# Kernel optimization log

Measured on AMD Instinct MI355X. Metric: run time of the kernel, lower is better.

The kernel has to match this reference:

```python
import jax, jax.numpy as jnp
import numpy as np

N = 50000
E = 500000
H = 128


def _linear(x, w, b):
    # torch nn.Linear: y = x @ W.T + b, W is [out, in]
    return x @ w.T + b


def _layer(x, h, edge_index, w0_w, w0_b, wl_w, wl_b, w1_w, w1_b):
    # PyG MessagePassing(aggr='add', flow='target_to_source'):
    # x_j = h[edge_index[1]], scatter-add into edge_index[0], dim_size = N
    msg = h[edge_index[1]]                               # [E, H] gather
    aggr = jax.ops.segment_sum(msg, edge_index[0], num_segments=h.shape[0])  # [N, H]
    return _linear(aggr, wl_w, wl_b) + _linear(h, w0_w, w0_b) + _linear(x, w1_w, w1_b)


def setup_inputs() -> dict:
    key = jax.random.key(0)
    ks = jax.random.split(key, 12)
    wscale = 0.05
    return {
        "x_a": jax.random.normal(ks[0], (N, H), jnp.float32),
        "x_b": jax.random.normal(ks[1], (N, H), jnp.float32),
        "edge_ab": jax.random.randint(ks[2], (2, E), 0, N, jnp.int32),
        "edge_ba": jax.random.randint(ks[3], (2, E), 0, N, jnp.int32),
        "conv0_w0_w": jax.random.normal(ks[4], (H, H), jnp.float32) * wscale,
        "conv0_w0_b": jnp.zeros((H,), jnp.float32),
        "conv0_wl_w": jax.random.normal(ks[5], (H, H), jnp.float32) * wscale,
        "conv0_wl_b": jnp.zeros((H,), jnp.float32),
        "conv0_w1_w": jax.random.normal(ks[6], (H, H), jnp.float32) * wscale,
        "conv0_w1_b": jnp.zeros((H,), jnp.float32),
        "conv1_w0_w": jax.random.normal(ks[7], (H, H), jnp.float32) * wscale,
        "conv1_w0_b": jnp.zeros((H,), jnp.float32),
        "conv1_wl_w": jax.random.normal(ks[8], (H, H), jnp.float32) * wscale,
        "conv1_wl_b": jnp.zeros((H,), jnp.float32),
        "conv1_w1_w": jax.random.normal(ks[9], (H, H), jnp.float32) * wscale,
        "conv1_w1_b": jnp.zeros((H,), jnp.float32),
        "out_w": jax.random.normal(ks[10], (H, H), jnp.float32) * wscale,
        "out_b": jnp.zeros((H,), jnp.float32),
    }


def reference(x_a, x_b, edge_ab, edge_ba,
              conv0_w0_w, conv0_w0_b, conv0_wl_w, conv0_wl_b, conv0_w1_w, conv0_w1_b,
              conv1_w0_w, conv1_w0_b, conv1_wl_w, conv1_wl_b, conv1_w1_w, conv1_w1_b,
              out_w, out_b):
    # metapath = [(a, r1, b), (b, r2, a)], loop over reversed(metapath):
    # iter 0: conv_idx=1, edge (b, r2, a), dst='a'
    h_a = jax.nn.relu(_layer(x_a, x_a, edge_ba,
                             conv1_w0_w, conv1_w0_b, conv1_wl_w, conv1_wl_b, conv1_w1_w, conv1_w1_b))
    # iter 1: conv_idx=0, edge (a, r1, b), dst='b'
    h_b = jax.nn.relu(_layer(x_b, x_b, edge_ab,
                             conv0_w0_w, conv0_w0_b, conv0_wl_w, conv0_wl_b, conv0_w1_w, conv0_w1_b))
    # start_type = 'a'
    return _linear(h_a, out_w, out_b)
```

## Files before the change

kernel.cpp:

```cpp
#include <hip/hip_runtime.h>
#include <hip/hip_bf16.h>

#define NN 50000
#define NE 500000
#define HD 128
#define CAP 128
#define PREP_B 24
#define ZCUR_B ((NN + 255) / 256)
#define ZAGGR_B 6250
#define K1_B (PREP_B + ZCUR_B + ZAGGR_B)
#define FILLB_B ((NE + 255) / 256)
#define XCONV_B 3125
#define K2_B (FILLB_B + XCONV_B)

typedef __bf16 bf16;
typedef __attribute__((ext_vector_type(8))) __bf16 bf16x8;
typedef __attribute__((ext_vector_type(4))) float floatx4;

__device__ inline float u2f(unsigned int lo16) {
    union { unsigned int i; float f; } c; c.i = lo16 << 16; return c.f;
}

__device__ inline bf16x8 cvt8(floatx4 a, floatx4 b) {
    bf16x8 r;
#pragma unroll
    for (int j = 0; j < 4; j++) { r[j] = (bf16)a[j]; r[j + 4] = (bf16)b[j]; }
    return r;
}

__device__ inline void split8(const floatx4 f0, const floatx4 f1, bf16x8& hi, bf16x8& lo) {
#pragma unroll
    for (int j = 0; j < 4; j++) {
        float a = f0[j]; bf16 h = (bf16)a; hi[j] = h; lo[j] = (bf16)(a - (float)h);
        float b = f1[j]; bf16 g = (bf16)b; hi[j + 4] = g; lo[j + 4] = (bf16)(b - (float)g);
    }
}

__device__ inline bf16x8 zero8() {
    bf16x8 v;
#pragma unroll
    for (int j = 0; j < 8; j++) v[j] = (bf16)0.f;
    return v;
}

__global__ __launch_bounds__(256) void k_setup1(
    const float* __restrict__ wl, const float* __restrict__ w0, const float* __restrict__ w1,
    const float* __restrict__ bl, const float* __restrict__ b0, const float* __restrict__ b1,
    const float* __restrict__ ow, const float* __restrict__ ob,
    bf16* __restrict__ wlb, bf16* __restrict__ w01b, bf16* __restrict__ owb,
    float* __restrict__ bias1, float* __restrict__ bias2,
    float* __restrict__ aggr, int* __restrict__ cur, int tier)
{
    const int b = blockIdx.x, tid = threadIdx.x;
    if (b < PREP_B) {
        int g = b * 256 + tid;
        int m = g >> 11, off = (g & 2047) << 3;
        if (m == 0) {
            const floatx4 a = *(const floatx4*)(wl + off);
            const floatx4 c = *(const floatx4*)(wl + off + 4);
            *(bf16x8*)(wlb + off) = cvt8(a, c);
        } else if (m == 1) {
            floatx4 a = *(const floatx4*)(w0 + off);
            floatx4 c = *(const floatx4*)(w0 + off + 4);
            const floatx4 d = *(const floatx4*)(w1 + off);
            const floatx4 e = *(const floatx4*)(w1 + off + 4);
#pragma unroll
            for (int j = 0; j < 4; j++) { a[j] += d[j]; c[j] += e[j]; }
            *(bf16x8*)(w01b + off) = cvt8(a, c);
        } else {
            const floatx4 a = *(const floatx4*)(ow + off);
            const floatx4 c = *(const floatx4*)(ow + off + 4);
            *(bf16x8*)(owb + off) = cvt8(a, c);
        }
        if (g < 128) bias1[g] = bl[g] + b0[g] + b1[g];
        else if (g < 256) bias2[g - 128] = ob[g - 128];
    } else if (b < PREP_B + ZCUR_B) {
        if (tier >= 1) {
            int i = (b - PREP_B) * 256 + tid;
            if (i < NN) cur[i] = 0;
        }
    } else {
        int i = (b - PREP_B - ZCUR_B) * 256 + tid;
        floatx4 z = {0.f, 0.f, 0.f, 0.f};
        ((floatx4*)aggr)[i] = z;
    }
}

__global__ __launch_bounds__(256) void k_setup2(
    const int* __restrict__ edge, const float* __restrict__ x,
    int* __restrict__ cur, int* __restrict__ bucket, float* __restrict__ aggr,
    bf16* __restrict__ xb)
{
    const int b = blockIdx.x, tid = threadIdx.x;
    if (b < FILLB_B) {
        int e = b * 256 + tid;
        if (e >= NE) return;
        int dst = edge[e];
        int src = edge[NE + e];
        int pos = atomicAdd(&cur[dst], 1);
        if (pos < CAP) {
            bucket[dst * CAP + pos] = src;
        } else {
            const float* xr = x + (size_t)src * HD;
            float* ar = aggr + (size_t)dst * HD;
            for (int c = 0; c < HD; c++) unsafeAtomicAdd(ar + c, xr[c]);
        }
    } else {
        int off = ((b - FILLB_B) * 256 + tid) << 3;
        const floatx4 a = *(const floatx4*)(x + off);
        const floatx4 c = *(const floatx4*)(x + off + 4);
        *(bf16x8*)(xb + off) = cvt8(a, c);
    }
}

__global__ __launch_bounds__(256) void k_aggr(const bf16* __restrict__ xb,
                                              const int* __restrict__ cur,
                                              const int* __restrict__ bucket,
                                              float* __restrict__ aggr) {
    const int gw   = (blockIdx.x * 256 + threadIdx.x) >> 6;
    const int lane = threadIdx.x & 63;
    const int quad = lane >> 4;
    const int ln   = lane & 15;
    const int node = gw * 4 + quad;
    const bool ok  = node < NN;

    float acc[8] = {0.f, 0.f, 0.f, 0.f, 0.f, 0.f, 0.f, 0.f};
    int deg = 0, n = 0;
    const int* bk = bucket;
    if (ok) {
        deg = cur[node];
        n = (deg < CAP) ? deg : CAP;
        bk = bucket + node * CAP;
        if (deg > CAP) {
            const floatx4 s0 = *(const floatx4*)(aggr + node * HD + ln * 8);
            const floatx4 s1 = *(const floatx4*)(aggr + node * HD + ln * 8 + 4);
#pragma unroll
            for (int j = 0; j < 4; j++) { acc[j] = s0[j]; acc[4 + j] = s1[j]; }
        }
    }

    int t = 0;
    for (; t + 3 < n; t += 4) {
        int s0 = bk[t], s1 = bk[t + 1], s2 = bk[t + 2], s3 = bk[t + 3];
        const uint4 v0 = *(const uint4*)(xb + s0 * HD + ln * 8);
        const uint4 v1 = *(const uint4*)(xb + s1 * HD + ln * 8);
        const uint4 v2 = *(const uint4*)(xb + s2 * HD + ln * 8);
        const uint4 v3 = *(const uint4*)(xb + s3 * HD + ln * 8);
        const unsigned int u0[4] = {v0.x, v0.y, v0.z, v0.w};
        const unsigned int u1[4] = {v1.x, v1.y, v1.z, v1.w};
        const unsigned int u2[4] = {v2.x, v2.y, v2.z, v2.w};
        const unsigned int u3[4] = {v3.x, v3.y, v3.z, v3.w};
#pragma unroll
        for (int j = 0; j < 4; j++) {
            acc[2 * j]     += u2f(u0[j] & 0xffff) + u2f(u1[j] & 0xffff)
                            + u2f(u2[j] & 0xffff) + u2f(u3[j] & 0xffff);
            acc[2 * j + 1] += u2f(u0[j] >> 16) + u2f(u1[j] >> 16)
                            + u2f(u2[j] >> 16) + u2f(u3[j] >> 16);
        }
    }
    for (; t < n; t++) {
        const uint4 v = *(const uint4*)(xb + bk[t] * HD + ln * 8);
        const unsigned int u[4] = {v.x, v.y, v.z, v.w};
#pragma unroll
        for (int j = 0; j < 4; j++) {
            acc[2 * j]     += u2f(u[j] & 0xffff);
            acc[2 * j + 1] += u2f(u[j] >> 16);
        }
    }

    if (ok) {
        floatx4 o0, o1;
#pragma unroll
        for (int j = 0; j < 4; j++) { o0[j] = acc[j]; o1[j] = acc[4 + j]; }
        *(floatx4*)(aggr + node * HD + ln * 8) = o0;
        *(floatx4*)(aggr + node * HD + ln * 8 + 4) = o1;
    }
}

__global__ __launch_bounds__(256) void k_scatter(const float* __restrict__ x,
                                                 const int* __restrict__ edge,
                                                 float* __restrict__ aggr) {
    int tid = blockIdx.x * 256 + threadIdx.x;
    int e = tid >> 5;
    int c = (tid & 31) << 2;
    int dst = edge[e];
    int src = edge[NE + e];
    const floatx4 v = *(const floatx4*)(x + src * HD + c);
    float* ap = aggr + dst * HD + c;
    unsafeAtomicAdd(ap + 0, v[0]);
    unsafeAtomicAdd(ap + 1, v[1]);
    unsafeAtomicAdd(ap + 2, v[2]);
    unsafeAtomicAdd(ap + 3, v[3]);
}

__global__ __launch_bounds__(256) void k_gemm12(
    const float* __restrict__ aggr, const float* __restrict__ x, const bf16* __restrict__ xb,
    int use_xb,
    const bf16* __restrict__ wlb, const bf16* __restrict__ w01b, const bf16* __restrict__ owb,
    const float* __restrict__ bias1, const float* __restrict__ bias2,
    float* __restrict__ out)
{
    __shared__ bf16 sA[128 * 136];
    __shared__ bf16 sB[128 * 136];
    __shared__ float b1_s[128], b2_s[128];
    float* tp = (float*)sB;
    const int tid = threadIdx.x;

#pragma unroll
    for (int it = 0; it < 8; it++) {
        int i = tid + it * 256;
        int r = i >> 4;
        int o = (i & 15) << 3;
        *(bf16x8*)(sA + r * 136 + o) = *(const bf16x8*)(wlb  + r * 128 + o);
        *(bf16x8*)(sB + r * 136 + o) = *(const bf16x8*)(w01b + r * 128 + o);
    }
    if (tid < 128) { b1_s[tid] = bias1[tid]; b2_s[tid] = bias2[tid]; }
    __syncthreads();

    const int lane = tid & 63;
    const int wv   = tid >> 6;
    const int ln   = lane & 15;
    const int quad = lane >> 4;
    const int row0 = blockIdx.x * 64 + wv * 16;
    const int arow = row0 + ln;
    const bool aok = arow < NN;

    floatx4 acc[8] = {};

#pragma unroll
    for (int kc = 0; kc < 4; kc++) {
        const int k0 = kc * 32 + quad * 8;
        bf16x8 a_hi = zero8(), a_lo = zero8(), a_x = zero8();
        if (aok) {
            const floatx4 f0 = *(const floatx4*)(aggr + arow * 128 + k0);
            const floatx4 f1 = *(const floatx4*)(aggr + arow * 128 + k0 + 4);
            split8(f0, f1, a_hi, a_lo);
            if (use_xb) {
                a_x = *(const bf16x8*)(xb + arow * 128 + k0);
            } else {
                const floatx4 g0 = *(const floatx4*)(x + arow * 128 + k0);
                const floatx4 g1 = *(const floatx4*)(x + arow * 128 + k0 + 4);
                a_x = cvt8(g0, g1);
            }
        }
#pragma unroll
        for (int nc = 0; nc < 8; nc++) {
            const bf16x8 bw  = *(const bf16x8*)(sA + (nc * 16 + ln) * 136 + k0);
            const bf16x8 bw2 = *(const bf16x8*)(sB + (nc * 16 + ln) * 136 + k0);
            acc[nc] = __builtin_amdgcn_mfma_f32_16x16x32_bf16(a_hi, bw,  acc[nc], 0, 0, 0);
            acc[nc] = __builtin_amdgcn_mfma_f32_16x16x32_bf16(a_lo, bw,  acc[nc], 0, 0, 0);
            acc[nc] = __builtin_amdgcn_mfma_f32_16x16x32_bf16(a_x,  bw2, acc[nc], 0, 0, 0);
        }
    }
    __syncthreads();

#pragma unroll
    for (int it = 0; it < 8; it++) {
        int i = tid + it * 256;
        int r = i >> 4;
        int o = (i & 15) << 3;
        *(bf16x8*)(sA + r * 136 + o) = *(const bf16x8*)(owb + r * 128 + o);
    }
#pragma unroll
    for (int nc = 0; nc < 8; nc++) {
        const int col = nc * 16 + ln;
        const float bv = b1_s[col];
#pragma unroll
        for (int r = 0; r < 4; r++) {
            float v = acc[nc][r] + bv;
            tp[wv * 2112 + (quad * 4 + r) * 132 + col] = (v > 0.f ? v : 0.f);
        }
        acc[nc][0] = acc[nc][1] = acc[nc][2] = acc[nc][3] = 0.f;
    }
    __syncthreads();

#pragma unroll
    for (int kc = 0; kc < 4; kc++) {
        const int k0 = kc * 32 + quad * 8;
        const floatx4 f0 = *(const floatx4*)(tp + wv * 2112 + ln * 132 + k0);
        const floatx4 f1 = *(const floatx4*)(tp + wv * 2112 + ln * 132 + k0 + 4);
        bf16x8 a_hi, a_lo;
        split8(f0, f1, a_hi, a_lo);
#pragma unroll
        for (int nc = 0; nc < 8; nc++) {
            const bf16x8 bw = *(const bf16x8*)(sA + (nc * 16 + ln) * 136 + k0);
            acc[nc] = __builtin_amdgcn_mfma_f32_16x16x32_bf16(a_hi, bw, acc[nc], 0, 0, 0);
            acc[nc] = __builtin_amdgcn_mfma_f32_16x16x32_bf16(a_lo, bw, acc[nc], 0, 0, 0);
        }
    }

#pragma unroll
    for (int nc = 0; nc < 8; nc++) {
        const int col = nc * 16 + ln;
        const float bv = b2_s[col];
#pragma unroll
        for (int r = 0; r < 4; r++) {
            const int row = row0 + quad * 4 + r;
            if (row < NN) out[row * 128 + col] = acc[nc][r] + bv;
        }
    }
}

extern "C" void kernel_launch(void* const* d_in, const int* in_sizes, int n_in,
                              void* d_out, int out_size, void* d_ws, size_t ws_size,
                              hipStream_t stream) {
    const float* x_a     = (const float*)d_in[0];
    const int*   edge_ba = (const int*)d_in[3];
    const float* c1_w0_w = (const float*)d_in[10];
    const float* c1_w0_b = (const float*)d_in[11];
    const float* c1_wl_w = (const float*)d_in[12];
    const float* c1_wl_b = (const float*)d_in[13];
    const float* c1_w1_w = (const float*)d_in[14];
    const float* c1_w1_b = (const float*)d_in[15];
    const float* out_w   = (const float*)d_in[16];
    const float* out_b   = (const float*)d_in[17];

    char* p = (char*)d_ws;
    float* aggr  = (float*)p;   p += (size_t)NN * HD * 4;
    bf16*  wlb   = (bf16*)p;    p += 32768;
    bf16*  w01b  = (bf16*)p;    p += 32768;
    bf16*  owb   = (bf16*)p;    p += 32768;
    float* bias1 = (float*)p;   p += 512;
    float* bias2 = (float*)p;   p += 512;
    const size_t WS_FALL = (size_t)(p - (char*)d_ws);
    int*   cur    = (int*)p;    p += 200704;
    int*   bucket = (int*)p;    p += (size_t)NN * CAP * 4;
    bf16*  xb     = (bf16*)p;   p += (size_t)NN * HD * 2;
    const size_t WS_BUCKET = (size_t)(p - (char*)d_ws);

    const int tier = (ws_size >= WS_BUCKET) ? 1 : 0;

    k_setup1<<<K1_B, 256, 0, stream>>>(c1_wl_w, c1_w0_w, c1_w1_w,
                                       c1_wl_b, c1_w0_b, c1_w1_b,
                                       out_w, out_b,
                                       wlb, w01b, owb, bias1, bias2,
                                       aggr, cur, tier);

    if (tier) {
        k_setup2<<<K2_B, 256, 0, stream>>>(edge_ba, x_a, cur, bucket, aggr, xb);
        k_aggr  <<<3125, 256, 0, stream>>>(xb, cur, bucket, aggr);
    } else {
        k_scatter<<<NE * 32 / 256, 256, 0, stream>>>(x_a, edge_ba, aggr);
    }

    k_gemm12<<<(NN + 63) / 64, 256, 0, stream>>>(aggr, x_a, xb, tier,
                                                 wlb, w01b, owb, bias1, bias2,
                                                 (float*)d_out);
}
```

Before: 197.3 us.

## Fuse neighbor aggregation into GEMM kernel and drop float aggr buffer

Removes the separate aggregation kernel and instead has each GEMM thread gather its node's bucketed neighbor rows from the bf16 copy of x directly into registers before the MFMA stage. Overflow edges beyond the bucket capacity are recorded in a list and scanned, replacing atomic adds into a float aggregate. This avoids zeroing, writing and re-reading the large fp32 aggregation buffer and one kernel launch, at the cost of per-lane serial gathers with lower memory-level parallelism and a potentially slow overflow scan.

```diff
diff --git a/kernel.cpp b/kernel.cpp
--- a/kernel.cpp
+++ b/kernel.cpp
@@ -8,7 +8,6 @@
 #define PREP_B 24
 #define ZCUR_B ((NN + 255) / 256)
 #define ZAGGR_B 6250
-#define K1_B (PREP_B + ZCUR_B + ZAGGR_B)
 #define FILLB_B ((NE + 255) / 256)
 #define XCONV_B 3125
 #define K2_B (FILLB_B + XCONV_B)
@@ -41,6 +40,13 @@
 #pragma unroll
     for (int j = 0; j < 8; j++) v[j] = (bf16)0.f;
     return v;
+}
+
+__device__ inline void addrow(floatx4& f0, floatx4& f1, const uint4 v) {
+    f0[0] += u2f(v.x & 0xffff); f0[1] += u2f(v.x >> 16);
+    f0[2] += u2f(v.y & 0xffff); f0[3] += u2f(v.y >> 16);
+    f1[0] += u2f(v.z & 0xffff); f1[1] += u2f(v.z >> 16);
+    f1[2] += u2f(v.w & 0xffff); f1[3] += u2f(v.w >> 16);
 }
 
 __global__ __launch_bounds__(256) void k_setup1(
@@ -49,7 +55,7 @@
     const float* __restrict__ ow, const float* __restrict__ ob,
     bf16* __restrict__ wlb, bf16* __restrict__ w01b, bf16* __restrict__ owb,
     float* __restrict__ bias1, float* __restrict__ bias2,
-    float* __restrict__ aggr, int* __restrict__ cur, int tier)
+    float* __restrict__ aggr, int* __restrict__ cur, int* __restrict__ ovf_cnt, int tier)
 {
     const int b = blockIdx.x, tid = threadIdx.x;
     if (b < PREP_B) {
@@ -78,6 +84,7 @@
         if (tier >= 1) {
             int i = (b - PREP_B) * 256 + tid;
             if (i < NN) cur[i] = 0;
+            if (b == PREP_B && tid == 0) *ovf_cnt = 0;
         }
     } else {
         int i = (b - PREP_B - ZCUR_B) * 256 + tid;
@@ -88,7 +95,8 @@
 
 __global__ __launch_bounds__(256) void k_setup2(
     const int* __restrict__ edge, const float* __restrict__ x,
-    int* __restrict__ cur, int* __restrict__ bucket, float* __restrict__ aggr,
+    int* __restrict__ cur, int* __restrict__ bucket,
+    int* __restrict__ ovf_cnt, int* __restrict__ ovf,
     bf16* __restrict__ xb)
 {
     const int b = blockIdx.x, tid = threadIdx.x;
@@ -101,79 +109,15 @@
         if (pos < CAP) {
             bucket[dst * CAP + pos] = src;
         } else {
-            const float* xr = x + (size_t)src * HD;
-            float* ar = aggr + (size_t)dst * HD;
-            for (int c = 0; c < HD; c++) unsafeAtomicAdd(ar + c, xr[c]);
+            int oi = atomicAdd(ovf_cnt, 1);
+            ovf[2 * oi] = dst;
+            ovf[2 * oi + 1] = src;
         }
     } else {
         int off = ((b - FILLB_B) * 256 + tid) << 3;
         const floatx4 a = *(const floatx4*)(x + off);
         const floatx4 c = *(const floatx4*)(x + off + 4);
         *(bf16x8*)(xb + off) = cvt8(a, c);
-    }
-}
-
-__global__ __launch_bounds__(256) void k_aggr(const bf16* __restrict__ xb,
-                                              const int* __restrict__ cur,
-                                              const int* __restrict__ bucket,
-                                              float* __restrict__ aggr) {
-    const int gw   = (blockIdx.x * 256 + threadIdx.x) >> 6;
-    const int lane = threadIdx.x & 63;
-    const int quad = lane >> 4;
-    const int ln   = lane & 15;
-    const int node = gw * 4 + quad;
-    const bool ok  = node < NN;
-
-    float acc[8] = {0.f, 0.f, 0.f, 0.f, 0.f, 0.f, 0.f, 0.f};
-    int deg = 0, n = 0;
-    const int* bk = bucket;
-    if (ok) {
-        deg = cur[node];
-        n = (deg < CAP) ? deg : CAP;
-        bk = bucket + node * CAP;
-        if (deg > CAP) {
-            const floatx4 s0 = *(const floatx4*)(aggr + node * HD + ln * 8);
-            const floatx4 s1 = *(const floatx4*)(aggr + node * HD + ln * 8 + 4);
-#pragma unroll
-            for (int j = 0; j < 4; j++) { acc[j] = s0[j]; acc[4 + j] = s1[j]; }
-        }
-    }
-
-    int t = 0;
-    for (; t + 3 < n; t += 4) {
-        int s0 = bk[t], s1 = bk[t + 1], s2 = bk[t + 2], s3 = bk[t + 3];
-        const uint4 v0 = *(const uint4*)(xb + s0 * HD + ln * 8);
-        const uint4 v1 = *(const uint4*)(xb + s1 * HD + ln * 8);
-        const uint4 v2 = *(const uint4*)(xb + s2 * HD + ln * 8);
-        const uint4 v3 = *(const uint4*)(xb + s3 * HD + ln * 8);
-        const unsigned int u0[4] = {v0.x, v0.y, v0.z, v0.w};
-        const unsigned int u1[4] = {v1.x, v1.y, v1.z, v1.w};
-        const unsigned int u2[4] = {v2.x, v2.y, v2.z, v2.w};
-        const unsigned int u3[4] = {v3.x, v3.y, v3.z, v3.w};
-#pragma unroll
-        for (int j = 0; j < 4; j++) {
-            acc[2 * j]     += u2f(u0[j] & 0xffff) + u2f(u1[j] & 0xffff)
-                            + u2f(u2[j] & 0xffff) + u2f(u3[j] & 0xffff);
-            acc[2 * j + 1] += u2f(u0[j] >> 16) + u2f(u1[j] >> 16)
-                            + u2f(u2[j] >> 16) + u2f(u3[j] >> 16);
-        }
-    }
-    for (; t < n; t++) {
-        const uint4 v = *(const uint4*)(xb + bk[t] * HD + ln * 8);
-        const unsigned int u[4] = {v.x, v.y, v.z, v.w};
-#pragma unroll
-        for (int j = 0; j < 4; j++) {
-            acc[2 * j]     += u2f(u[j] & 0xffff);
-            acc[2 * j + 1] += u2f(u[j] >> 16);
-        }
-    }
-
-    if (ok) {
-        floatx4 o0, o1;
-#pragma unroll
-        for (int j = 0; j < 4; j++) { o0[j] = acc[j]; o1[j] = acc[4 + j]; }
-        *(floatx4*)(aggr + node * HD + ln * 8) = o0;
-        *(floatx4*)(aggr + node * HD + ln * 8 + 4) = o1;
     }
 }
 
@@ -193,9 +137,11 @@
     unsafeAtomicAdd(ap + 3, v[3]);
 }
 
-__global__ __launch_bounds__(256) void k_gemm12(
+__global__ __launch_bounds__(256) void k_fused(
     const float* __restrict__ aggr, const float* __restrict__ x, const bf16* __restrict__ xb,
-    int use_xb,
+    int tier,
+    const int* __restrict__ cur, const int* __restrict__ bucket,
+    const int* __restrict__ ovf_cnt, const int* __restrict__ ovf,
     const bf16* __restrict__ wlb, const bf16* __restrict__ w01b, const bf16* __restrict__ owb,
     const float* __restrict__ bias1, const float* __restrict__ bias2,
     float* __restrict__ out)
@@ -215,7 +161,6 @@
         *(bf16x8*)(sB + r * 136 + o) = *(const bf16x8*)(w01b + r * 128 + o);
     }
     if (tid < 128) { b1_s[tid] = bias1[tid]; b2_s[tid] = bias2[tid]; }
-    __syncthreads();
 
     const int lane = tid & 63;
     const int wv   = tid >> 6;
@@ -224,22 +169,81 @@
     const int row0 = blockIdx.x * 64 + wv * 16;
     const int arow = row0 + ln;
     const bool aok = arow < NN;
+    const int q8   = quad * 8;
+
+    floatx4 ag0[4] = {};
+    floatx4 ag1[4] = {};
+
+    if (tier) {
+        int deg = 0, n = 0;
+        if (aok) { deg = cur[arow]; n = (deg < CAP) ? deg : CAP; }
+        const int* bk = bucket + (size_t)arow * CAP;
+        int t = 0;
+        for (; t + 1 < n; t += 2) {
+            const int s0 = bk[t], s1 = bk[t + 1];
+            const bf16* r0 = xb + (size_t)s0 * HD + q8;
+            const bf16* r1 = xb + (size_t)s1 * HD + q8;
+            const uint4 a0 = *(const uint4*)(r0);
+            const uint4 a1 = *(const uint4*)(r0 + 32);
+            const uint4 a2 = *(const uint4*)(r0 + 64);
+            const uint4 a3 = *(const uint4*)(r0 + 96);
+            const uint4 c0 = *(const uint4*)(r1);
+            const uint4 c1 = *(const uint4*)(r1 + 32);
+            const uint4 c2 = *(const uint4*)(r1 + 64);
+            const uint4 c3 = *(const uint4*)(r1 + 96);
+            addrow(ag0[0], ag1[0], a0); addrow(ag0[1], ag1[1], a1);
+            addrow(ag0[2], ag1[2], a2); addrow(ag0[3], ag1[3], a3);
+            addrow(ag0[0], ag1[0], c0); addrow(ag0[1], ag1[1], c1);
+            addrow(ag0[2], ag1[2], c2); addrow(ag0[3], ag1[3], c3);
+        }
+        if (t < n) {
+            const int s0 = bk[t];
+            const bf16* r0 = xb + (size_t)s0 * HD + q8;
+            const uint4 a0 = *(const uint4*)(r0);
+            const uint4 a1 = *(const uint4*)(r0 + 32);
+            const uint4 a2 = *(const uint4*)(r0 + 64);
+            const uint4 a3 = *(const uint4*)(r0 + 96);
+            addrow(ag0[0], ag1[0], a0); addrow(ag0[1], ag1[1], a1);
+            addrow(ag0[2], ag1[2], a2); addrow(ag0[3], ag1[3], a3);
+        }
+        if (deg > CAP) {
+            const int m = *ovf_cnt;
+            for (int i = 0; i < m; i++) {
+                if (ovf[2 * i] == arow) {
+                    const bf16* r0 = xb + (size_t)ovf[2 * i + 1] * HD + q8;
+                    const uint4 a0 = *(const uint4*)(r0);
+                    const uint4 a1 = *(const uint4*)(r0 + 32);
+                    const uint4 a2 = *(const uint4*)(r0 + 64);
+                    const uint4 a3 = *(const uint4*)(r0 + 96);
+                    addrow(ag0[0], ag1[0], a0); addrow(ag0[1], ag1[1], a1);
+                    addrow(ag0[2], ag1[2], a2); addrow(ag0[3], ag1[3], a3);
+                }
+            }
+        }
+    } else if (aok) {
+#pragma unroll
+        for (int kc = 0; kc < 4; kc++) {
+            ag0[kc] = *(const floatx4*)(aggr + (size_t)arow * HD + kc * 32 + q8);
+            ag1[kc] = *(const floatx4*)(aggr + (size_t)arow * HD + kc * 32 + q8 + 4);
+        }
+    }
+
+    __syncthreads();
 
     floatx4 acc[8] = {};
 
 #pragma unroll
     for (int kc = 0; kc < 4; kc++) {
-        const int k0 = kc * 32 + quad * 8;
-        bf16x8 a_hi = zero8(), a_lo = zero8(), a_x = zero8();
+        const int k0 = kc * 32 + q8;
+        bf16x8 a_hi, a_lo;
+        split8(ag0[kc], ag1[kc], a_hi, a_lo);
+        bf16x8 a_x = zero8();
         if (aok) {
-            const floatx4 f0 = *(const floatx4*)(aggr + arow * 128 + k0);
-            const floatx4 f1 = *(const floatx4*)(aggr + arow * 128 + k0 + 4);
-            split8(f0, f1, a_hi, a_lo);
-            if (use_xb) {
-                a_x = *(const bf16x8*)(xb + arow * 128 + k0);
+            if (tier) {
+                a_x = *(const bf16x8*)(xb + (size_t)arow * HD + k0);
             } else {
-                const floatx4 g0 = *(const floatx4*)(x + arow * 128 + k0);
-                const floatx4 g1 = *(const floatx4*)(x + arow * 128 + k0 + 4);
+                const floatx4 g0 = *(const floatx4*)(x + (size_t)arow * HD + k0);
+                const floatx4 g1 = *(const floatx4*)(x + (size_t)arow * HD + k0 + 4);
                 a_x = cvt8(g0, g1);
             }
         }
@@ -276,7 +280,7 @@
 
 #pragma unroll
     for (int kc = 0; kc < 4; kc++) {
-        const int k0 = kc * 32 + quad * 8;
+        const int k0 = kc * 32 + q8;
         const floatx4 f0 = *(const floatx4*)(tp + wv * 2112 + ln * 132 + k0);
         const floatx4 f1 = *(const floatx4*)(tp + wv * 2112 + ln * 132 + k0 + 4);
         bf16x8 a_hi, a_lo;
@@ -326,24 +330,28 @@
     int*   cur    = (int*)p;    p += 200704;
     int*   bucket = (int*)p;    p += (size_t)NN * CAP * 4;
     bf16*  xb     = (bf16*)p;   p += (size_t)NN * HD * 2;
+    int*   ovf_cnt= (int*)p;    p += 256;
+    int*   ovf    = (int*)p;    p += (size_t)NE * 2 * 4;
     const size_t WS_BUCKET = (size_t)(p - (char*)d_ws);
+    (void)WS_FALL;
 
     const int tier = (ws_size >= WS_BUCKET) ? 1 : 0;
 
-    k_setup1<<<K1_B, 256, 0, stream>>>(c1_wl_w, c1_w0_w, c1_w1_w,
-                                       c1_wl_b, c1_w0_b, c1_w1_b,
-                                       out_w, out_b,
-                                       wlb, w01b, owb, bias1, bias2,
-                                       aggr, cur, tier);
+    const int k1_grid = tier ? (PREP_B + ZCUR_B) : (PREP_B + ZCUR_B + ZAGGR_B);
+    k_setup1<<<k1_grid, 256, 0, stream>>>(c1_wl_w, c1_w0_w, c1_w1_w,
+                                          c1_wl_b, c1_w0_b, c1_w1_b,
+                                          out_w, out_b,
+                                          wlb, w01b, owb, bias1, bias2,
+                                          aggr, cur, ovf_cnt, tier);
 
     if (tier) {
-        k_setup2<<<K2_B, 256, 0, stream>>>(edge_ba, x_a, cur, bucket, aggr, xb);
-        k_aggr  <<<3125, 256, 0, stream>>>(xb, cur, bucket, aggr);
+        k_setup2<<<K2_B, 256, 0, stream>>>(edge_ba, x_a, cur, bucket, ovf_cnt, ovf, xb);
     } else {
         k_scatter<<<NE * 32 / 256, 256, 0, stream>>>(x_a, edge_ba, aggr);
     }
 
-    k_gemm12<<<(NN + 63) / 64, 256, 0, stream>>>(aggr, x_a, xb, tier,
-                                                 wlb, w01b, owb, bias1, bias2,
-                                                 (float*)d_out);
-}
+    k_fused<<<(NN + 63) / 64, 256, 0, stream>>>(aggr, x_a, xb, tier,
+                                                cur, bucket, ovf_cnt, ovf,
+                                                wlb, w01b, owb, bias1, bias2,
+                                                (float*)d_out);
+}
```

New measurement: 192.9 us. -2.2%, faster.
